# Kernel tuning notes

Measured on AMD Instinct MI355X. Metric: run time of the kernel, lower is better.

Reference implementation:

```python
import jax, jax.numpy as jnp
import numpy as np

PACK = 8  # 32 bits / 4 bits per value


def _unpack_int4(packed):
    # packed: [..., O//8] int32 -> [..., O] int32 nibbles in [0, 16)
    shifts = jnp.arange(PACK, dtype=jnp.int32) * 4
    nib = (packed[..., None] >> shifts) & jnp.int32(0xF)
    return nib.reshape(*packed.shape[:-1], packed.shape[-1] * PACK)


def setup_inputs() -> dict:
    key = jax.random.key(0)
    k1, k2, k3, k4 = jax.random.split(key, 4)
    I, O, GS = 4096, 11008, 128
    G = I // GS
    x = jax.random.normal(k1, (4096, I), dtype=jnp.float32)
    qweight = jax.random.randint(k2, (I, O // PACK), -2**31, 2**31 - 1, dtype=jnp.int32)
    scales = jax.random.uniform(k3, (G, O), dtype=jnp.float32) * 0.01 + 1e-3
    qzeros = jax.random.randint(k4, (G, O // PACK), -2**31, 2**31 - 1, dtype=jnp.int32)
    return {"x": x, "qweight": qweight, "scales": scales, "qzeros": qzeros, "group_size": GS}


def reference(x, qweight, scales, qzeros, group_size):
    I = qweight.shape[0]
    O = qweight.shape[1] * PACK
    G = I // group_size
    w_int = _unpack_int4(qweight)                       # [I, O] int32
    z_int = _unpack_int4(qzeros)                        # [G, O] int32
    # dequant: (w - zero_of_group) * scale_of_group
    w_grp = w_int.reshape(G, group_size, O).astype(jnp.float32)
    w_deq = (w_grp - z_int[:, None, :].astype(jnp.float32)) * scales[:, None, :]
    w_deq = w_deq.reshape(I, O)                         # [I, O] float32
    return x @ w_deq                                    # [N, O]
```

## Files before the change

kernel.cpp:

```cpp
#include <hip/hip_runtime.h>
#include <hip/hip_bf16.h>
#include <stdint.h>

#define M_DIM 4096
#define K_DIM 4096
#define N_DIM 11008
#define OPACK (N_DIM / 8)
#define GSZ   128

#define M_TILES (M_DIM / 128)
#define N_TILES (N_DIM / 128)
#define K_ITERS (K_DIM / 32)

typedef __attribute__((ext_vector_type(8))) short short8;
typedef __attribute__((ext_vector_type(4))) float floatx4;
typedef __attribute__((ext_vector_type(4))) unsigned int uintx4;

static __device__ __forceinline__ unsigned short f32_to_bf16_rne(float f) {
    union { float f; unsigned int u; } c; c.f = f;
    unsigned int u = c.u;
    u += 0x7fffu + ((u >> 16) & 1u);
    return (unsigned short)(u >> 16);
}

static __device__ __forceinline__ void load16_lds(const void* gptr, void* lptr) {
    __builtin_amdgcn_global_load_lds(
        (__attribute__((address_space(1))) void*)gptr,
        (__attribute__((address_space(3))) void*)lptr,
        16, 0, 0);
}

__global__ __launch_bounds__(256)
void convert_x_kernel(const float* __restrict__ x, unsigned short* __restrict__ xb) {
    const int idx = (blockIdx.x * 256 + threadIdx.x) * 8;
    floatx4 v0 = *(const floatx4*)(x + idx);
    floatx4 v1 = *(const floatx4*)(x + idx + 4);
    unsigned short r[8];
#pragma unroll
    for (int i = 0; i < 4; i++) {
        r[i]     = f32_to_bf16_rne(v0[i]);
        r[4 + i] = f32_to_bf16_rne(v1[i]);
    }
    *(uintx4*)(xb + idx) = *(const uintx4*)r;
}

__global__ __launch_bounds__(256)
void dequant_kernel(const int* __restrict__ qweight, const float* __restrict__ scales,
                    const int* __restrict__ qzeros, unsigned short* __restrict__ Wt) {
    const int o  = blockIdx.x * 256 + threadIdx.x;
    const int i0 = blockIdx.y * 32;
    const int g  = i0 >> 7;
    const int op = o >> 3;
    const int sh = (o & 7) * 4;
    const int z  = (qzeros[g * OPACK + op] >> sh) & 15;
    const float s = scales[g * N_DIM + o];
    unsigned short buf[32];
#pragma unroll
    for (int k = 0; k < 32; k++) {
        const int q   = qweight[(i0 + k) * OPACK + op];
        const float w = (float)(((q >> sh) & 15) - z) * s;
        buf[k] = f32_to_bf16_rne(w);
    }
    uintx4* dst = (uintx4*)(Wt + (size_t)o * K_DIM + i0);
    const uintx4* src = (const uintx4*)buf;
#pragma unroll
    for (int t = 0; t < 4; t++) dst[t] = src[t];
}

__global__ __launch_bounds__(256)
void gemm_kernel(const unsigned short* __restrict__ X,
                 const unsigned short* __restrict__ Wt,
                 float* __restrict__ C) {
    __shared__ short As[2][128 * 32];
    __shared__ short Bs[2][128 * 32];

    const int tid  = threadIdx.x;
    const int wave = tid >> 6;
    const int lane = tid & 63;

    const int pid    = blockIdx.x;
    const int xcd    = pid & 7;
    const int loc    = pid >> 3;
    const int m_tile = xcd * 4 + (loc & 3);
    const int n_tile = loc >> 2;
    const int n0 = n_tile * 128;
    const int m0 = m_tile * 128;

    const int wm = (wave >> 1) * 64;
    const int wn = (wave & 1) * 64;

    const int srow = tid >> 2;
    const int scol = (tid & 3) * 8;
    const unsigned short* Ap0 = X  + (m0 + srow) * K_DIM + scol;
    const unsigned short* Ap1 = X  + (m0 + srow + 64) * K_DIM + scol;
    const unsigned short* Bp0 = Wt + (n0 + srow) * K_DIM + scol;
    const unsigned short* Bp1 = Wt + (n0 + srow + 64) * K_DIM + scol;
    const int l0 = tid * 16;
    const int l1 = (tid + 256) * 16;

    floatx4 acc[4][4] = {};

    const int frow  = lane & 15;
    const int kfrag = (lane >> 4) * 8;

    load16_lds(Ap0, (char*)As[0] + l0);
    load16_lds(Ap1, (char*)As[0] + l1);
    load16_lds(Bp0, (char*)Bs[0] + l0);
    load16_lds(Bp1, (char*)Bs[0] + l1);
    __syncthreads();

    for (int it = 0; it < K_ITERS; ++it) {
        const int cur = it & 1;
        const int nxt = cur ^ 1;
        if (it + 1 < K_ITERS) {
            const int kn = (it + 1) * 32;
            load16_lds(Ap0 + kn, (char*)As[nxt] + l0);
            load16_lds(Ap1 + kn, (char*)As[nxt] + l1);
            load16_lds(Bp0 + kn, (char*)Bs[nxt] + l0);
            load16_lds(Bp1 + kn, (char*)Bs[nxt] + l1);
        }

        const short* Ac = As[cur];
        const short* Bc = Bs[cur];
        short8 a[4], b[4];
#pragma unroll
        for (int t = 0; t < 4; t++) {
            a[t] = *(const short8*)(Ac + (wm + t * 16 + frow) * 32 + kfrag);
            b[t] = *(const short8*)(Bc + (wn + t * 16 + frow) * 32 + kfrag);
        }
#pragma unroll
        for (int i = 0; i < 4; i++)
#pragma unroll
            for (int j = 0; j < 4; j++)
                acc[i][j] = __builtin_amdgcn_mfma_f32_16x16x32_bf16(a[i], b[j], acc[i][j], 0, 0, 0);

        __syncthreads();
    }

    const int crow = (lane >> 4) * 4;
    const int ccol = lane & 15;
#pragma unroll
    for (int i = 0; i < 4; i++) {
#pragma unroll
        for (int j = 0; j < 4; j++) {
            float* Cp = C + (m0 + wm + i * 16 + crow) * N_DIM + (n0 + wn + j * 16 + ccol);
#pragma unroll
            for (int r = 0; r < 4; r++)
                __builtin_nontemporal_store(acc[i][j][r], Cp + r * N_DIM);
        }
    }
}

extern "C" void kernel_launch(void* const* d_in, const int* in_sizes, int n_in,
                              void* d_out, int out_size, void* d_ws, size_t ws_size,
                              hipStream_t stream) {
    const float* x       = (const float*)d_in[0];
    const int*   qweight = (const int*)d_in[1];
    const float* scales  = (const float*)d_in[2];
    const int*   qzeros  = (const int*)d_in[3];
    float* out = (float*)d_out;

    unsigned short* Xb = (unsigned short*)d_ws;
    unsigned short* Wt = (unsigned short*)((char*)d_ws + (size_t)M_DIM * K_DIM * 2);

    convert_x_kernel<<<(M_DIM * K_DIM) / (256 * 8), 256, 0, stream>>>(x, Xb);
    dequant_kernel<<<dim3(N_DIM / 256, K_DIM / 32), 256, 0, stream>>>(qweight, scales, qzeros, Wt);
    gemm_kernel<<<M_TILES * N_TILES, 256, 0, stream>>>(Xb, Wt, out);
}
```

Measured before the change: 722.9 us.

## Use 256x256 GEMM tiles with 8 waves, 4-stage LDS pipeline and swizzle

The GEMM moves from 128x128 tiles with 4 waves to 256x256 tiles with 8 waves (512 threads). A 4-deep global_load_lds ring is driven by an explicit ping-pong phase schedule that uses manual s_waitcnt, s_barrier, setprio and sched_barrier. An XOR swizzle on the LDS layout is meant to avoid bank conflicts, and the block-to-XCD mapping is remapped for L2 reuse. The dequant kernel now handles 64 rows of K per thread. Each A/B byte loaded now feeds more MFMA work, at the cost of 128 KB of LDS per block, higher register pressure, and fragile hand-tuned synchronisation.

```diff
diff --git a/kernel.cpp b/kernel.cpp
--- a/kernel.cpp
+++ b/kernel.cpp
@@ -8,9 +8,7 @@
 #define OPACK (N_DIM / 8)
 #define GSZ   128
 
-#define M_TILES (M_DIM / 128)
-#define N_TILES (N_DIM / 128)
-#define K_ITERS (K_DIM / 32)
+#define NIT 32
 
 typedef __attribute__((ext_vector_type(8))) short short8;
 typedef __attribute__((ext_vector_type(4))) float floatx4;
@@ -48,15 +46,15 @@
 void dequant_kernel(const int* __restrict__ qweight, const float* __restrict__ scales,
                     const int* __restrict__ qzeros, unsigned short* __restrict__ Wt) {
     const int o  = blockIdx.x * 256 + threadIdx.x;
-    const int i0 = blockIdx.y * 32;
+    const int i0 = blockIdx.y * 64;
     const int g  = i0 >> 7;
     const int op = o >> 3;
     const int sh = (o & 7) * 4;
     const int z  = (qzeros[g * OPACK + op] >> sh) & 15;
     const float s = scales[g * N_DIM + o];
-    unsigned short buf[32];
+    unsigned short buf[64];
 #pragma unroll
-    for (int k = 0; k < 32; k++) {
+    for (int k = 0; k < 64; k++) {
         const int q   = qweight[(i0 + k) * OPACK + op];
         const float w = (float)(((q >> sh) & 15) - z) * s;
         buf[k] = f32_to_bf16_rne(w);
@@ -64,89 +62,120 @@
     uintx4* dst = (uintx4*)(Wt + (size_t)o * K_DIM + i0);
     const uintx4* src = (const uintx4*)buf;
 #pragma unroll
-    for (int t = 0; t < 4; t++) dst[t] = src[t];
+    for (int t = 0; t < 8; t++) dst[t] = src[t];
 }
 
-__global__ __launch_bounds__(256)
+
+#define STAGE_A(KB, RG) do {                                   \
+    const char* g_ = ApS + (size_t)(KB) * 64;                  \
+    char* l_ = (char*)lds_a[RG] + tid * 16;                    \
+    load16_lds(g_, l_);                                        \
+    load16_lds(g_ + (1u << 20), l_ + 8192);                    \
+} while (0)
+
+#define STAGE_B(KB, RG) do {                                   \
+    const char* g_ = BpS + (size_t)(KB) * 64;                  \
+    char* l_ = (char*)lds_b[RG] + tid * 16;                    \
+    load16_lds(g_, l_);                                        \
+    load16_lds(g_ + (1u << 20), l_ + 8192);                    \
+} while (0)
+
+#define VM_NONE ((void)0)
+#define VM_TILE do {                                                        \
+    if (more) { asm volatile("s_waitcnt vmcnt(6)" ::: "memory"); }          \
+    else      { asm volatile("s_waitcnt vmcnt(0)" ::: "memory"); }          \
+} while (0)
+
+#define PHASE(B_, KS_, H_, VMW_, ...) do {                                           \
+    const short* Ar_ = &lds_a[(B_) * 2 + (KS_)][a_off + (H_) * 2048];                \
+    short8 av_[4];                                                                   \
+    _Pragma("unroll")                                                                \
+    for (int f_ = 0; f_ < 4; ++f_) av_[f_] = *(const short8*)(Ar_ + f_ * 512);       \
+    if ((H_) == 0) {                                                                 \
+        const short* Br_ = &lds_b[(B_) * 2 + (KS_)][b_off];                          \
+        _Pragma("unroll")                                                            \
+        for (int n_ = 0; n_ < 4; ++n_) bv[n_] = *(const short8*)(Br_ + n_ * 512);    \
+    }                                                                                \
+    __VA_ARGS__;                                                                     \
+    VMW_;                                                                            \
+    __builtin_amdgcn_s_barrier();                                                    \
+    asm volatile("s_waitcnt lgkmcnt(0)" ::: "memory");                               \
+    __builtin_amdgcn_sched_barrier(0);                                               \
+    __builtin_amdgcn_s_setprio(1);                                                   \
+    _Pragma("unroll")                                                                \
+    for (int f_ = 0; f_ < 4; ++f_)                                                   \
+        _Pragma("unroll")                                                            \
+        for (int n_ = 0; n_ < 4; ++n_)                                               \
+            acc[(H_) * 4 + f_][n_] = __builtin_amdgcn_mfma_f32_16x16x32_bf16(        \
+                av_[f_], bv[n_], acc[(H_) * 4 + f_][n_], 0, 0, 0);                   \
+    __builtin_amdgcn_s_setprio(0);                                                   \
+    __builtin_amdgcn_s_barrier();                                                    \
+} while (0)
+
+__global__ __launch_bounds__(512, 2)
 void gemm_kernel(const unsigned short* __restrict__ X,
                  const unsigned short* __restrict__ Wt,
                  float* __restrict__ C) {
-    __shared__ short As[2][128 * 32];
-    __shared__ short Bs[2][128 * 32];
+    __shared__ __align__(16) short lds_a[4][8192];
+    __shared__ __align__(16) short lds_b[4][8192];
 
     const int tid  = threadIdx.x;
     const int wave = tid >> 6;
     const int lane = tid & 63;
+    const int wm   = wave >> 2;
+    const int wn   = wave & 3;
 
     const int pid    = blockIdx.x;
-    const int xcd    = pid & 7;
-    const int loc    = pid >> 3;
-    const int m_tile = xcd * 4 + (loc & 3);
-    const int n_tile = loc >> 2;
-    const int n0 = n_tile * 128;
-    const int m0 = m_tile * 128;
+    const int L      = (pid & 7) * 86 + (pid >> 3);
+    const int m_tile = L & 15;
+    const int n_tile = L >> 4;
+    const int m0 = m_tile * 256;
+    const int n0 = n_tile * 256;
 
-    const int wm = (wave >> 1) * 64;
-    const int wn = (wave & 1) * 64;
+    const int row_l = tid >> 2;
+    const int cl    = (tid & 3) ^ ((tid >> 3) & 3);
+    const char* ApS = (const char*)X  + ((size_t)(m0 + row_l) << 13) + (cl << 4);
+    const char* BpS = (const char*)Wt + ((size_t)(n0 + row_l) << 13) + (cl << 4);
 
-    const int srow = tid >> 2;
-    const int scol = (tid & 3) * 8;
-    const unsigned short* Ap0 = X  + (m0 + srow) * K_DIM + scol;
-    const unsigned short* Ap1 = X  + (m0 + srow + 64) * K_DIM + scol;
-    const unsigned short* Bp0 = Wt + (n0 + srow) * K_DIM + scol;
-    const unsigned short* Bp1 = Wt + (n0 + srow + 64) * K_DIM + scol;
-    const int l0 = tid * 16;
-    const int l1 = (tid + 256) * 16;
+    const int l15 = lane & 15;
+    const int kcs = (lane >> 4) ^ ((lane >> 1) & 3);
+    const int a_off = (wm * 128 + l15) * 32 + kcs * 8;
+    const int b_off = (wn * 64  + l15) * 32 + kcs * 8;
 
-    floatx4 acc[4][4] = {};
+    floatx4 acc[8][4] = {};
+    short8 bv[4];
 
-    const int frow  = lane & 15;
-    const int kfrag = (lane >> 4) * 8;
+    STAGE_B(0, 0); STAGE_A(0, 0);
+    STAGE_B(1, 1); STAGE_A(1, 1);
+    STAGE_B(2, 2); STAGE_A(2, 2);
+    STAGE_B(3, 3);
+    asm volatile("s_waitcnt vmcnt(6)" ::: "memory");
+    __builtin_amdgcn_s_barrier();
 
-    load16_lds(Ap0, (char*)As[0] + l0);
-    load16_lds(Ap1, (char*)As[0] + l1);
-    load16_lds(Bp0, (char*)Bs[0] + l0);
-    load16_lds(Bp1, (char*)Bs[0] + l1);
-    __syncthreads();
-
-    for (int it = 0; it < K_ITERS; ++it) {
-        const int cur = it & 1;
-        const int nxt = cur ^ 1;
-        if (it + 1 < K_ITERS) {
-            const int kn = (it + 1) * 32;
-            load16_lds(Ap0 + kn, (char*)As[nxt] + l0);
-            load16_lds(Ap1 + kn, (char*)As[nxt] + l1);
-            load16_lds(Bp0 + kn, (char*)Bs[nxt] + l0);
-            load16_lds(Bp1 + kn, (char*)Bs[nxt] + l1);
-        }
-
-        const short* Ac = As[cur];
-        const short* Bc = Bs[cur];
-        short8 a[4], b[4];
-#pragma unroll
-        for (int t = 0; t < 4; t++) {
-            a[t] = *(const short8*)(Ac + (wm + t * 16 + frow) * 32 + kfrag);
-            b[t] = *(const short8*)(Bc + (wn + t * 16 + frow) * 32 + kfrag);
-        }
-#pragma unroll
-        for (int i = 0; i < 4; i++)
-#pragma unroll
-            for (int j = 0; j < 4; j++)
-                acc[i][j] = __builtin_amdgcn_mfma_f32_16x16x32_bf16(a[i], b[j], acc[i][j], 0, 0, 0);
-
-        __syncthreads();
+#pragma unroll 1
+    for (int i = 0; i < NIT; ++i) {
+        const int  kb4  = 4 * i;
+        const bool more = (i + 1 < NIT);
+        PHASE(0, 0, 0, VM_NONE, STAGE_A(kb4 + 3, 3));
+        PHASE(0, 0, 1, VM_NONE, if (more) STAGE_B(kb4 + 4, 0));
+        PHASE(0, 1, 0, VM_NONE, if (more) STAGE_A(kb4 + 4, 0));
+        PHASE(0, 1, 1, VM_TILE, if (more) STAGE_B(kb4 + 5, 1));
+        PHASE(1, 0, 0, VM_NONE, if (more) STAGE_A(kb4 + 5, 1));
+        PHASE(1, 0, 1, VM_NONE, if (more) STAGE_B(kb4 + 6, 2));
+        PHASE(1, 1, 0, VM_NONE, if (more) STAGE_A(kb4 + 6, 2));
+        PHASE(1, 1, 1, VM_TILE, if (more) STAGE_B(kb4 + 7, 3));
     }
 
     const int crow = (lane >> 4) * 4;
-    const int ccol = lane & 15;
 #pragma unroll
-    for (int i = 0; i < 4; i++) {
+    for (int f = 0; f < 8; ++f) {
 #pragma unroll
-        for (int j = 0; j < 4; j++) {
-            float* Cp = C + (m0 + wm + i * 16 + crow) * N_DIM + (n0 + wn + j * 16 + ccol);
+        for (int n = 0; n < 4; ++n) {
+            float* Cp = C + (size_t)(m0 + wm * 128 + f * 16 + crow) * N_DIM
+                          + (n0 + wn * 64 + n * 16 + l15);
 #pragma unroll
-            for (int r = 0; r < 4; r++)
-                __builtin_nontemporal_store(acc[i][j][r], Cp + r * N_DIM);
+            for (int r = 0; r < 4; ++r)
+                __builtin_nontemporal_store(acc[f][n][r], Cp + (size_t)r * N_DIM);
         }
     }
 }
@@ -164,6 +193,6 @@
     unsigned short* Wt = (unsigned short*)((char*)d_ws + (size_t)M_DIM * K_DIM * 2);
 
     convert_x_kernel<<<(M_DIM * K_DIM) / (256 * 8), 256, 0, stream>>>(x, Xb);
-    dequant_kernel<<<dim3(N_DIM / 256, K_DIM / 32), 256, 0, stream>>>(qweight, scales, qzeros, Wt);
-    gemm_kernel<<<M_TILES * N_TILES, 256, 0, stream>>>(Xb, Wt, out);
+    dequant_kernel<<<dim3(N_DIM / 256, K_DIM / 64), 256, 0, stream>>>(qweight, scales, qzeros, Wt);
+    gemm_kernel<<<(M_DIM / 256) * (N_DIM / 256), 512, 0, stream>>>(Xb, Wt, out);
 }
```

After: 620.3 us. 14.2% less time.
